# Kernel tuning notes

Hardware: AMD Instinct MI355X
Metric: run time of the kernel (lower is better)

Reference implementation:

```python
import jax, jax.numpy as jnp
import numpy as np

NQ, NK = 32, 128          # block height / width (AF3 local attention)
INF = 1.0e9
EPS = 1e-5


def _ln(x, w=None, b=None):
    m = jnp.mean(x, axis=-1, keepdims=True)
    v = jnp.var(x, axis=-1, keepdims=True)
    y = (x - m) * jax.lax.rsqrt(v + EPS)
    if w is not None:
        y = y * w
    if b is not None:
        y = y + b
    return y


def _key_idx(N):
    # For query block i, keys cover a window of NK atoms centered on the block.
    nb = N // NQ
    start = np.arange(nb)[:, None] * NQ - (NK - NQ) // 2
    idx = start + np.arange(NK)[None, :]          # [nb, NK]
    valid = ((idx >= 0) & (idx < N)).astype(np.float32)
    return np.clip(idx, 0, N - 1), valid


def setup_inputs() -> dict:
    key = jax.random.key(0)
    ks = iter(jax.random.split(key, 32))
    B, N, C, CZ, H, CH, CS = 4, 8192, 128, 16, 4, 32, 128
    nb = N // NQ
    nrm = lambda sh, sc=0.02: jax.random.normal(next(ks), sh, jnp.float32) * sc
    return dict(
        a=nrm((B, N, C), 1.0),
        z=nrm((B, nb, NQ, NK, CZ), 1.0),
        s=nrm((B, N, CS), 1.0),
        mask=jnp.ones((B, N), jnp.float32),
        ln_s_q_w=jnp.ones((CS,), jnp.float32),
        Wg_q=nrm((CS, C)), bg_q=jnp.zeros((C,), jnp.float32), Wb_q=nrm((CS, C)),
        ln_s_k_w=jnp.ones((CS,), jnp.float32),
        Wg_k=nrm((CS, C)), bg_k=jnp.zeros((C,), jnp.float32), Wb_k=nrm((CS, C)),
        ln_z_w=jnp.ones((CZ,), jnp.float32), ln_z_b=jnp.zeros((CZ,), jnp.float32),
        W_z=nrm((CZ, H)),
        Wq=nrm((C, H * CH)), Wk=nrm((C, H * CH)), Wv=nrm((C, H * CH)),
        Wg=nrm((C, H * CH)), bg=jnp.ones((H * CH,), jnp.float32),
        Wo=nrm((H * CH, C)), bo=jnp.zeros((C,), jnp.float32),
        W_ado=nrm((CS, C)), b_ado=jnp.full((C,), -2.0, jnp.float32),
    )


def reference(a, z, s, mask,
              ln_s_q_w, Wg_q, bg_q, Wb_q,
              ln_s_k_w, Wg_k, bg_k, Wb_k,
              ln_z_w, ln_z_b, W_z,
              Wq, Wk, Wv, Wg, bg, Wo, bo,
              W_ado, b_ado):
    B, N, C = a.shape
    H = W_z.shape[1]
    CH = Wq.shape[1] // H
    nb = N // NQ
    idx, valid = _key_idx(N)

    # --- block inputs ---
    a_q = a.reshape(B, nb, NQ, C)            # [B, nb, NQ, C]
    a_k = a[:, idx]                          # [B, nb, NK, C]
    q_mask = mask.reshape(B, nb, NQ)
    k_mask = mask[:, idx] * valid            # [B, nb, NK]
    pair_mask = q_mask[..., :, None] * k_mask[..., None, :]   # [B, nb, NQ, NK]
    mask_bias = (INF * (pair_mask - 1.0))[..., None, :, :]     # [B, nb, 1, NQ, NK]

    # --- pair bias from z ---
    zb = _ln(z, ln_z_w, ln_z_b) @ W_z        # [B, nb, NQ, NK, H]
    zb = jnp.moveaxis(zb, -1, -3)            # [B, nb, H, NQ, NK]

    # --- AdaLN conditioning ---
    s_q = s.reshape(B, nb, NQ, -1)
    s_k = s[:, idx]
    sqn = _ln(s_q, ln_s_q_w)
    skn = _ln(s_k, ln_s_k_w)
    aq = jax.nn.sigmoid(sqn @ Wg_q + bg_q) * _ln(a_q) + sqn @ Wb_q
    ak = jax.nn.sigmoid(skn @ Wg_k + bg_k) * _ln(a_k) + skn @ Wb_k

    # --- blocked attention with pair bias ---
    scale = 1.0 / np.sqrt(CH).astype(np.float32)
    q = (aq @ Wq).reshape(B, nb, NQ, H, CH) * scale
    k = (ak @ Wk).reshape(B, nb, NK, H, CH)
    v = (ak @ Wv).reshape(B, nb, NK, H, CH)
    logits = jnp.einsum('bnqhc,bnkhc->bnhqk', q, k) + mask_bias + zb
    attn = jax.nn.softmax(logits, axis=-1)
    o = jnp.einsum('bnhqk,bnkhc->bnqhc', attn, v)
    g = jax.nn.sigmoid(aq @ Wg + bg).reshape(B, nb, NQ, H, CH)
    o = (g * o).reshape(B, nb, NQ, H * CH)
    out = (o @ Wo + bo).reshape(B, N, C)[:, :N, :]

    # --- AdaLN-Zero output gate ---
    out = jax.nn.sigmoid(s @ W_ado + b_ado) * out
    return out
```

## Files before the change

### kernel.cpp

```cpp
#include <hip/hip_runtime.h>
#include <cstdint>
#include <cstddef>

#define B_ 4
#define N_ 8192
#define C_ 128
#define NB_ 256
#define EPS_ 1e-5f

typedef unsigned int u32;
typedef unsigned short u16;

typedef short bf16x8 __attribute__((ext_vector_type(8)));
typedef float f32x4 __attribute__((ext_vector_type(4)));
union U16x8 { uint4 u4; bf16x8 v; };

__device__ __forceinline__ float bf2f(u16 v){ union{u32 i; float f;} x; x.i = ((u32)v)<<16; return x.f; }
__device__ __forceinline__ u16 f2bf(float f){ union{float f; u32 i;} x; x.f=f; u32 r = x.i + 0x7fffu + ((x.i>>16)&1u); return (u16)(r>>16); }
__device__ __forceinline__ u32 pk2(float a, float b){ return (u32)f2bf(a) | ((u32)f2bf(b)<<16); }
__device__ __forceinline__ float sigm(float x){ return 1.f/(1.f+__expf(-x)); }

__global__ void k0_prep(const float* __restrict__ Wgq, const float* __restrict__ Wbq,
                        const float* __restrict__ Wgk, const float* __restrict__ Wbk,
                        const float* __restrict__ Wado, const float* __restrict__ Wq_,
                        const float* __restrict__ Wg_, const float* __restrict__ Wk_,
                        const float* __restrict__ Wv_, const float* __restrict__ Wo_,
                        const float* __restrict__ lnsqw, const float* __restrict__ lnskw,
                        const float* __restrict__ lnzw, const float* __restrict__ lnzb,
                        const float* __restrict__ Wz,
                        u16* __restrict__ PW, float* __restrict__ AUX)
{
  if (blockIdx.x < 80) {
    int gid = blockIdx.x*256 + threadIdx.x;
    int mat = gid >> 11;
    int rem = gid & 2047;
    int ks = rem >> 9;
    int rem2 = rem & 511;
    int nt = rem2 >> 6;
    int lane = rem2 & 63;
    int kbase = ks*32 + (lane>>4)*8;
    int n = nt*16 + (lane&15);
    const float* W; int scmode = 0; float fixed = 1.f;
    switch (mat) {
      case 0: W = Wgq; scmode = 1; break;
      case 1: W = Wbq; scmode = 1; break;
      case 2: W = Wgk; scmode = 2; break;
      case 3: W = Wbk; scmode = 2; break;
      case 4: W = Wado; break;
      case 5: W = Wq_; fixed = 0.17677669529663687f; break;
      case 6: W = Wg_; break;
      case 7: W = Wk_; break;
      case 8: W = Wv_; break;
      default: W = Wo_; break;
    }
    u16 o[8];
    #pragma unroll
    for (int j=0;j<8;j++){
      int k = kbase + j;
      float sc = fixed;
      if (scmode == 1) sc *= lnsqw[k];
      else if (scmode == 2) sc *= lnskw[k];
      o[j] = f2bf(W[k*128 + n] * sc);
    }
    uint4 pk;
    pk.x = (u32)o[0] | ((u32)o[1]<<16); pk.y = (u32)o[2] | ((u32)o[3]<<16);
    pk.z = (u32)o[4] | ((u32)o[5]<<16); pk.w = (u32)o[6] | ((u32)o[7]<<16);
    *(uint4*)(PW + (size_t)gid*8) = pk;
  } else {
    int t = threadIdx.x;
    if (t < 128) {
      float s = 0.f;
      for (int k=0;k<128;k++) s += Wado[k*128 + t];
      AUX[t] = s;
    } else if (t < 192) {
      int h = (t-128) >> 4, c = (t-128) & 15;
      AUX[t] = lnzw[c] * Wz[c*4 + h];
    } else if (t < 196) {
      int h = t - 192;
      float s = 0.f;
      for (int c=0;c<16;c++) s += lnzb[c]*Wz[c*4 + h];
      AUX[t] = s;
    }
  }
}

__device__ __forceinline__ void mm_single(f32x4 acc[4][2], const u16* Abase, const u16* __restrict__ PW,
                                          int mat, int wave, int lane, int lq, int quad)
{
  #pragma unroll
  for (int ks=0; ks<4; ks++){
    U16x8 b0, b1;
    b0.u4 = *(const uint4*)(PW + (size_t)((((mat*4+ks)*8) + wave*2+0)*64 + lane)*8);
    b1.u4 = *(const uint4*)(PW + (size_t)((((mat*4+ks)*8) + wave*2+1)*64 + lane)*8);
    #pragma unroll
    for (int mt=0; mt<4; mt++){
      U16x8 a; a.u4 = *(const uint4*)(Abase + (mt*16+lq)*136 + ks*32 + quad*8);
      acc[mt][0] = __builtin_amdgcn_mfma_f32_16x16x32_bf16(a.v, b0.v, acc[mt][0], 0,0,0);
      acc[mt][1] = __builtin_amdgcn_mfma_f32_16x16x32_bf16(a.v, b1.v, acc[mt][1], 0,0,0);
    }
  }
}
__device__ __forceinline__ void mm_dual(f32x4 acc1[4][2], int m1, f32x4 acc2[4][2], int m2,
                                        const u16* Abase, const u16* __restrict__ PW,
                                        int wave, int lane, int lq, int quad)
{
  #pragma unroll
  for (int ks=0; ks<4; ks++){
    U16x8 b10, b11, b20, b21;
    b10.u4 = *(const uint4*)(PW + (size_t)((((m1*4+ks)*8) + wave*2+0)*64 + lane)*8);
    b11.u4 = *(const uint4*)(PW + (size_t)((((m1*4+ks)*8) + wave*2+1)*64 + lane)*8);
    b20.u4 = *(const uint4*)(PW + (size_t)((((m2*4+ks)*8) + wave*2+0)*64 + lane)*8);
    b21.u4 = *(const uint4*)(PW + (size_t)((((m2*4+ks)*8) + wave*2+1)*64 + lane)*8);
    #pragma unroll
    for (int mt=0; mt<4; mt++){
      U16x8 a; a.u4 = *(const uint4*)(Abase + (mt*16+lq)*136 + ks*32 + quad*8);
      acc1[mt][0] = __builtin_amdgcn_mfma_f32_16x16x32_bf16(a.v, b10.v, acc1[mt][0], 0,0,0);
      acc1[mt][1] = __builtin_amdgcn_mfma_f32_16x16x32_bf16(a.v, b11.v, acc1[mt][1], 0,0,0);
      acc2[mt][0] = __builtin_amdgcn_mfma_f32_16x16x32_bf16(a.v, b20.v, acc2[mt][0], 0,0,0);
      acc2[mt][1] = __builtin_amdgcn_mfma_f32_16x16x32_bf16(a.v, b21.v, acc2[mt][1], 0,0,0);
    }
  }
}
#define ZERO82(A) do{ _Pragma("unroll") for(int _m=0;_m<4;_m++){ A[_m][0]=(f32x4)(0.f); A[_m][1]=(f32x4)(0.f);} }while(0)

__global__ __launch_bounds__(256, 2)
void k1_proj(const float* __restrict__ ga, const float* __restrict__ gs,
             const float* __restrict__ bgq, const float* __restrict__ bgk,
             const float* __restrict__ bg, const float* __restrict__ bado,
             const u16* __restrict__ PW, const float* __restrict__ AUX,
             u16* __restrict__ Q, u16* __restrict__ K, u16* __restrict__ VT,
             u16* __restrict__ GT, u16* __restrict__ ADO)
{
  __shared__ char arena[52736];
  u16* SN  = (u16*)arena;
  u16* LNA = (u16*)(arena + 17408);
  u16* AQ  = (u16*)(arena + 34816);
  float* SSTAT = (float*)(arena + 52224);

  const int tid = (int)threadIdx.x;
  const int rowbase = (int)blockIdx.x * 64;
  const int b = rowbase >> 13;
  const int nb0 = rowbase & 8191;
  const int wave = tid >> 6, lane = tid & 63;
  const int lq = lane & 15, quad = lane >> 4;

  {
    const float* sbase = gs + (size_t)rowbase*128;
    const float* abase = ga + (size_t)rowbase*128;
    #pragma unroll 1
    for (int t=0;t<8;t++){
      int chunk = t*256 + tid;
      int row = chunk >> 5;
      int k4 = (chunk & 31) * 4;
      float4 vs = *(const float4*)(sbase + (size_t)chunk*4);
      float4 va = *(const float4*)(abase + (size_t)chunk*4);
      float sm = vs.x+vs.y+vs.z+vs.w, sq = vs.x*vs.x+vs.y*vs.y+vs.z*vs.z+vs.w*vs.w;
      float am = va.x+va.y+va.z+va.w, a2 = va.x*va.x+va.y*va.y+va.z*va.z+va.w*va.w;
      #pragma unroll
      for (int m=1;m<32;m<<=1){
        sm += __shfl_xor(sm,m,32); sq += __shfl_xor(sq,m,32);
        am += __shfl_xor(am,m,32); a2 += __shfl_xor(a2,m,32);
      }
      float smean = sm*(1.f/128.f);
      float svar  = sq*(1.f/128.f) - smean*smean;
      float srstd = rsqrtf(svar + EPS_);
      float amean = am*(1.f/128.f);
      float avar  = a2*(1.f/128.f) - amean*amean;
      float arstd = rsqrtf(avar + EPS_);
      *(uint2*)(SN + row*136 + k4) = make_uint2(
        pk2((vs.x-smean)*srstd,(vs.y-smean)*srstd), pk2((vs.z-smean)*srstd,(vs.w-smean)*srstd));
      *(uint2*)(LNA + row*136 + k4) = make_uint2(
        pk2((va.x-amean)*arstd,(va.y-amean)*arstd), pk2((va.z-amean)*arstd,(va.w-amean)*arstd));
      if ((tid & 31) == 0){
        SSTAT[row*2]   = smean;
        SSTAT[row*2+1] = (svar + EPS_)*srstd;
      }
    }
  }
  __syncthreads();

  const int cg0 = wave*32 + lq;
  const int cg1 = cg0 + 16;

  {
    f32x4 acc[4][2]; ZERO82(acc);
    mm_single(acc, SN, PW, 4, wave, lane, lq, quad);
    float cs0 = AUX[cg0], cs1 = AUX[cg1];
    float bb0 = bado[cg0], bb1 = bado[cg1];
    #pragma unroll
    for (int mt=0; mt<4; mt++){
      #pragma unroll
      for (int reg=0; reg<4; reg++){
        int row = mt*16 + quad*4 + reg;
        float mean = SSTAT[row*2], std = SSTAT[row*2+1];
        ADO[(size_t)(rowbase+row)*128 + cg0] = f2bf(sigm(std*acc[mt][0][reg] + mean*cs0 + bb0));
        ADO[(size_t)(rowbase+row)*128 + cg1] = f2bf(sigm(std*acc[mt][1][reg] + mean*cs1 + bb1));
      }
    }
  }

  {
    f32x4 aG[4][2], aB[4][2]; ZERO82(aG); ZERO82(aB);
    mm_dual(aG, 0, aB, 1, SN, PW, wave, lane, lq, quad);
    float bq0 = bgq[cg0], bq1 = bgq[cg1];
    #pragma unroll
    for (int mt=0; mt<4; mt++){
      #pragma unroll
      for (int reg=0; reg<4; reg++){
        int row = mt*16 + quad*4 + reg;
        float l0 = bf2f(LNA[row*136 + cg0]), l1 = bf2f(LNA[row*136 + cg1]);
        AQ[row*136 + cg0] = f2bf(sigm(aG[mt][0][reg]+bq0)*l0 + aB[mt][0][reg]);
        AQ[row*136 + cg1] = f2bf(sigm(aG[mt][1][reg]+bq1)*l1 + aB[mt][1][reg]);
      }
    }
  }

  {
    f32x4 aG[4][2], aB[4][2]; ZERO82(aG); ZERO82(aB);
    mm_dual(aG, 2, aB, 3, SN, PW, wave, lane, lq, quad);
    float bk0 = bgk[cg0], bk1 = bgk[cg1];
    #pragma unroll
    for (int mt=0; mt<4; mt++){
      #pragma unroll
      for (int reg=0; reg<4; reg++){
        int row = mt*16 + quad*4 + reg;
        float l0 = bf2f(LNA[row*136 + cg0]), l1 = bf2f(LNA[row*136 + cg1]);
        aG[mt][0][reg] = sigm(aG[mt][0][reg]+bk0)*l0 + aB[mt][0][reg];
        aG[mt][1][reg] = sigm(aG[mt][1][reg]+bk1)*l1 + aB[mt][1][reg];
      }
    }
    __syncthreads();
    #pragma unroll
    for (int mt=0; mt<4; mt++){
      #pragma unroll
      for (int reg=0; reg<4; reg++){
        int row = mt*16 + quad*4 + reg;
        SN[row*136 + cg0] = f2bf(aG[mt][0][reg]);
        SN[row*136 + cg1] = f2bf(aG[mt][1][reg]);
      }
    }
    __syncthreads();
  }

  {
    f32x4 aQ_[4][2], aG_[4][2]; ZERO82(aQ_); ZERO82(aG_);
    mm_dual(aQ_, 5, aG_, 6, AQ, PW, wave, lane, lq, quad);
    float bg0 = bg[cg0], bg1 = bg[cg1];
    #pragma unroll
    for (int mt=0; mt<4; mt++){
      #pragma unroll
      for (int reg=0; reg<4; reg++){
        int row = mt*16 + quad*4 + reg;
        Q[(size_t)(rowbase+row)*128 + cg0] = f2bf(aQ_[mt][0][reg]);
        Q[(size_t)(rowbase+row)*128 + cg1] = f2bf(aQ_[mt][1][reg]);
      }
      ushort4 p0, p1;
      p0.x = f2bf(sigm(aG_[mt][0][0]+bg0)); p0.y = f2bf(sigm(aG_[mt][0][1]+bg0));
      p0.z = f2bf(sigm(aG_[mt][0][2]+bg0)); p0.w = f2bf(sigm(aG_[mt][0][3]+bg0));
      p1.x = f2bf(sigm(aG_[mt][1][0]+bg1)); p1.y = f2bf(sigm(aG_[mt][1][1]+bg1));
      p1.z = f2bf(sigm(aG_[mt][1][2]+bg1)); p1.w = f2bf(sigm(aG_[mt][1][3]+bg1));
      int nloc = nb0 + mt*16 + quad*4;
      *(ushort4*)(GT + ((size_t)(b*128 + cg0))*N_ + nloc) = p0;
      *(ushort4*)(GT + ((size_t)(b*128 + cg1))*N_ + nloc) = p1;
    }
  }

  {
    f32x4 aK_[4][2], aV_[4][2]; ZERO82(aK_); ZERO82(aV_);
    mm_dual(aK_, 7, aV_, 8, SN, PW, wave, lane, lq, quad);
    #pragma unroll
    for (int mt=0; mt<4; mt++){
      #pragma unroll
      for (int reg=0; reg<4; reg++){
        int row = mt*16 + quad*4 + reg;
        K[(size_t)(rowbase+row)*128 + cg0] = f2bf(aK_[mt][0][reg]);
        K[(size_t)(rowbase+row)*128 + cg1] = f2bf(aK_[mt][1][reg]);
      }
      ushort4 p0, p1;
      p0.x = f2bf(aV_[mt][0][0]); p0.y = f2bf(aV_[mt][0][1]);
      p0.z = f2bf(aV_[mt][0][2]); p0.w = f2bf(aV_[mt][0][3]);
      p1.x = f2bf(aV_[mt][1][0]); p1.y = f2bf(aV_[mt][1][1]);
      p1.z = f2bf(aV_[mt][1][2]); p1.w = f2bf(aV_[mt][1][3]);
      int nloc = nb0 + mt*16 + quad*4;
      *(ushort4*)(VT + ((size_t)(b*128 + cg0))*N_ + nloc) = p0;
      *(ushort4*)(VT + ((size_t)(b*128 + cg1))*N_ + nloc) = p1;
    }
  }
}

__global__ __launch_bounds__(256, 3)
void k2_attn(const float* __restrict__ gz, const float* __restrict__ gmask,
             const float* __restrict__ bo,
             const u16* __restrict__ PW, const float* __restrict__ AUX,
             const u16* __restrict__ Q, const u16* __restrict__ K,
             const u16* __restrict__ VT, const u16* __restrict__ GT,
             const u16* __restrict__ ADO, float* __restrict__ gout)
{
  __shared__ char arena[44160];
  u16* ATTall = (u16*)arena;
  u16* GO     = (u16*)(arena + 34816);
  float* KMV  = (float*)(arena + 43520);
  float* QM   = (float*)(arena + 44032);

  const int i = (int)blockIdx.x, b = (int)blockIdx.y;
  const int tid = (int)threadIdx.x;
  const int wave = tid >> 6, lane = tid & 63;
  const int lq = lane & 15, quad = lane >> 4;
  const int h = wave;
  const int start = i*32 - 48;
  u16* ATT = ATTall + h*(32*136);

  if (tid < 128) {
    int raw = start + tid;
    int g = min(max(raw,0), N_-1);
    KMV[tid] = ((raw >= 0 && raw < N_) ? 1.f : 0.f) * gmask[(size_t)b*N_ + g];
  } else if (tid < 160) {
    QM[tid-128] = gmask[(size_t)b*N_ + i*32 + (tid-128)];
  }
  __syncthreads();

  f32x4 L[2][8];
  #pragma unroll
  for (int mt=0;mt<2;mt++) for (int nt=0;nt<8;nt++) L[mt][nt] = (f32x4)(0.f);
  {
    U16x8 aQ[2];
    #pragma unroll
    for (int mt=0;mt<2;mt++)
      aQ[mt].u4 = *(const uint4*)(Q + ((size_t)b*N_ + i*32 + mt*16 + lq)*128 + h*32 + quad*8);
    #pragma unroll
    for (int nt=0;nt<8;nt++){
      int kr = min(max(start + nt*16 + lq, 0), N_-1);
      U16x8 bk; bk.u4 = *(const uint4*)(K + ((size_t)b*N_ + kr)*128 + h*32 + quad*8);
      L[0][nt] = __builtin_amdgcn_mfma_f32_16x16x32_bf16(aQ[0].v, bk.v, L[0][nt], 0,0,0);
      L[1][nt] = __builtin_amdgcn_mfma_f32_16x16x32_bf16(aQ[1].v, bk.v, L[1][nt], 0,0,0);
    }
  }

  {
    float wz[16]; float wzt = 0.f;
    #pragma unroll
    for (int c=0;c<16;c++){ wz[c] = AUX[128 + h*16 + c]; wzt += wz[c]; }
    float wzc = AUX[192 + h];
    float kmvv[8];
    #pragma unroll
    for (int nt=0;nt<8;nt++) kmvv[nt] = KMV[nt*16 + lq];
    const float* zb0 = gz + (size_t)(b*NB_ + i)*32*128*16;
    #pragma unroll
    for (int mt=0;mt<2;mt++){
      #pragma unroll 1
      for (int reg=0;reg<4;reg++){
        int q = mt*16 + quad*4 + reg;
        float qm = QM[q];
        const float* zq = zb0 + (size_t)q*128*16 + lq*16;
        #pragma unroll 2
        for (int nt=0;nt<8;nt++){
          const float* zp = zq + nt*16*16;
          float4 z0 = *(const float4*)(zp);
          float4 z1 = *(const float4*)(zp+4);
          float4 z2 = *(const float4*)(zp+8);
          float4 z3 = *(const float4*)(zp+12);
          float zv[16] = {z0.x,z0.y,z0.z,z0.w, z1.x,z1.y,z1.z,z1.w,
                          z2.x,z2.y,z2.z,z2.w, z3.x,z3.y,z3.z,z3.w};
          float sm=0.f, sq=0.f, S=0.f;
          #pragma unroll
          for (int c=0;c<16;c++){ sm += zv[c]; sq = fmaf(zv[c],zv[c],sq); S = fmaf(zv[c],wz[c],S); }
          float mz = sm*(1.f/16.f);
          float rz = rsqrtf(sq*(1.f/16.f) - mz*mz + EPS_);
          float bias = 1000000000.0f*(qm*kmvv[nt] - 1.f);
          L[mt][nt][reg] += (S - mz*wzt)*rz + wzc + bias;
        }
      }
    }
  }

  #pragma unroll
  for (int mt=0;mt<2;mt++){
    #pragma unroll
    for (int reg=0;reg<4;reg++){
      float mx = -3.0e38f;
      #pragma unroll
      for (int nt=0;nt<8;nt++) mx = fmaxf(mx, L[mt][nt][reg]);
      mx = fmaxf(mx, __shfl_xor(mx,1,16));
      mx = fmaxf(mx, __shfl_xor(mx,2,16));
      mx = fmaxf(mx, __shfl_xor(mx,4,16));
      mx = fmaxf(mx, __shfl_xor(mx,8,16));
      float e[8]; float s = 0.f;
      #pragma unroll
      for (int nt=0;nt<8;nt++){ e[nt] = __expf(L[mt][nt][reg]-mx); s += e[nt]; }
      s += __shfl_xor(s,1,16);
      s += __shfl_xor(s,2,16);
      s += __shfl_xor(s,4,16);
      s += __shfl_xor(s,8,16);
      float inv = 1.f/s;
      int q = mt*16 + quad*4 + reg;
      #pragma unroll
      for (int nt=0;nt<8;nt++) ATT[q*136 + nt*16 + lq] = f2bf(e[nt]*inv);
    }
  }

  f32x4 O[2][2];
  O[0][0]=(f32x4)(0.f); O[0][1]=(f32x4)(0.f); O[1][0]=(f32x4)(0.f); O[1][1]=(f32x4)(0.f);
  #pragma unroll
  for (int ks=0;ks<4;ks++){
    U16x8 ba[2];
    #pragma unroll
    for (int nt=0;nt<2;nt++)
      ba[nt].u4 = *(const uint4*)(ATT + (nt*16+lq)*136 + ks*32 + quad*8);
    int kk = start + ks*32 + quad*8;
    kk = min(max(kk,0), N_-8);
    #pragma unroll
    for (int mt=0;mt<2;mt++){
      U16x8 av;
      av.u4 = *(const uint4*)(VT + ((size_t)(b*128 + h*32 + mt*16 + lq))*N_ + kk);
      O[mt][0] = __builtin_amdgcn_mfma_f32_16x16x32_bf16(av.v, ba[0].v, O[mt][0], 0,0,0);
      O[mt][1] = __builtin_amdgcn_mfma_f32_16x16x32_bf16(av.v, ba[1].v, O[mt][1], 0,0,0);
    }
  }

  #pragma unroll
  for (int mt=0;mt<2;mt++){
    #pragma unroll
    for (int nt=0;nt<2;nt++){
      int q = nt*16 + lq;
      int cb = h*32 + mt*16 + quad*4;
      float g0 = bf2f(GT[((size_t)(b*128 + cb+0))*N_ + i*32 + q]);
      float g1 = bf2f(GT[((size_t)(b*128 + cb+1))*N_ + i*32 + q]);
      float g2 = bf2f(GT[((size_t)(b*128 + cb+2))*N_ + i*32 + q]);
      float g3 = bf2f(GT[((size_t)(b*128 + cb+3))*N_ + i*32 + q]);
      ushort4 p;
      p.x = f2bf(g0*O[mt][nt][0]); p.y = f2bf(g1*O[mt][nt][1]);
      p.z = f2bf(g2*O[mt][nt][2]); p.w = f2bf(g3*O[mt][nt][3]);
      *(ushort4*)(GO + q*136 + cb) = p;
    }
  }
  __syncthreads();

  {
    f32x4 U[2][2];
    U[0][0]=(f32x4)(0.f); U[0][1]=(f32x4)(0.f); U[1][0]=(f32x4)(0.f); U[1][1]=(f32x4)(0.f);
    #pragma unroll
    for (int ks=0;ks<4;ks++){
      U16x8 b0, b1;
      b0.u4 = *(const uint4*)(PW + (size_t)((((9*4+ks)*8) + wave*2+0)*64 + lane)*8);
      b1.u4 = *(const uint4*)(PW + (size_t)((((9*4+ks)*8) + wave*2+1)*64 + lane)*8);
      #pragma unroll
      for (int mt=0;mt<2;mt++){
        U16x8 a; a.u4 = *(const uint4*)(GO + (mt*16+lq)*136 + ks*32 + quad*8);
        U[mt][0] = __builtin_amdgcn_mfma_f32_16x16x32_bf16(a.v, b0.v, U[mt][0], 0,0,0);
        U[mt][1] = __builtin_amdgcn_mfma_f32_16x16x32_bf16(a.v, b1.v, U[mt][1], 0,0,0);
      }
    }
    const int cg0 = wave*32 + lq, cg1 = cg0 + 16;
    float b00 = bo[cg0], b01 = bo[cg1];
    #pragma unroll
    for (int mt=0;mt<2;mt++){
      #pragma unroll
      for (int reg=0;reg<4;reg++){
        int q = mt*16 + quad*4 + reg;
        size_t rowoff = ((size_t)b*N_ + i*32 + q)*128;
        float ad0 = bf2f(ADO[rowoff + cg0]);
        float ad1 = bf2f(ADO[rowoff + cg1]);
        gout[rowoff + cg0] = ad0*(U[mt][0][reg] + b00);
        gout[rowoff + cg1] = ad1*(U[mt][1][reg] + b01);
      }
    }
  }
}

extern "C" void kernel_launch(void* const* d_in, const int* in_sizes, int n_in,
                              void* d_out, int out_size, void* d_ws, size_t ws_size,
                              hipStream_t stream) {
  (void)in_sizes; (void)n_in; (void)out_size; (void)ws_size;
  const float* ga    = (const float*)d_in[0];
  const float* gz    = (const float*)d_in[1];
  const float* gs    = (const float*)d_in[2];
  const float* gmask = (const float*)d_in[3];
  const float* lnsqw = (const float*)d_in[4];
  const float* Wgq   = (const float*)d_in[5];
  const float* bgq   = (const float*)d_in[6];
  const float* Wbq   = (const float*)d_in[7];
  const float* lnskw = (const float*)d_in[8];
  const float* Wgk   = (const float*)d_in[9];
  const float* bgk   = (const float*)d_in[10];
  const float* Wbk   = (const float*)d_in[11];
  const float* lnzw  = (const float*)d_in[12];
  const float* lnzb  = (const float*)d_in[13];
  const float* Wz    = (const float*)d_in[14];
  const float* Wq    = (const float*)d_in[15];
  const float* Wk    = (const float*)d_in[16];
  const float* Wv    = (const float*)d_in[17];
  const float* Wg    = (const float*)d_in[18];
  const float* bg    = (const float*)d_in[19];
  const float* Wo    = (const float*)d_in[20];
  const float* bo    = (const float*)d_in[21];
  const float* Wado  = (const float*)d_in[22];
  const float* bado  = (const float*)d_in[23];

  char* ws = (char*)d_ws;
  u16* Qb  = (u16*)(ws + 0);
  u16* Kb  = (u16*)(ws + 8388608);
  u16* VTb = (u16*)(ws + 16777216);
  u16* GTb = (u16*)(ws + 25165824);
  u16* ADOb= (u16*)(ws + 33554432);
  u16* PW  = (u16*)(ws + 41943040);
  float* AUX = (float*)(ws + 41943040 + 327680);

  k0_prep<<<81, 256, 0, stream>>>(Wgq, Wbq, Wgk, Wbk, Wado, Wq, Wg, Wk, Wv, Wo,
                                  lnsqw, lnskw, lnzw, lnzb, Wz, PW, AUX);
  k1_proj<<<512, 256, 0, stream>>>(ga, gs, bgq, bgk, bg, bado, PW, AUX,
                                   Qb, Kb, VTb, GTb, ADOb);
  k2_attn<<<dim3(NB_, B_), 256, 0, stream>>>(gz, gmask, bo, PW, AUX,
                                             Qb, Kb, VTb, GTb, ADOb, (float*)d_out);
}
```

Measured before the change: 551.8 us.

## Precompute pair bias with mask into bf16 buffer in prep kernel

Moves the z layernorm, W_z projection and mask bias out of the attention kernel into extra blocks of the prep kernel, which writes a bf16 per-head bias tensor [B,nb,H,NK,NQ]. The attention kernel then adds this bias with vectorized loads instead of re-reading 128 MB of fp32 z inside the softmax stage. The sigmoid gate is stored row-major instead of transposed, attention shared memory is reduced so occupancy can rise from 3 to 4 blocks, and the block index is remapped. The trade-off is an extra 32 MB bias write and read, plus bf16 rounding of the bias including the large mask term.

```diff
diff --git a/kernel.cpp b/kernel.cpp
--- a/kernel.cpp
+++ b/kernel.cpp
@@ -28,59 +28,113 @@
                         const float* __restrict__ lnsqw, const float* __restrict__ lnskw,
                         const float* __restrict__ lnzw, const float* __restrict__ lnzb,
                         const float* __restrict__ Wz,
-                        u16* __restrict__ PW, float* __restrict__ AUX)
+                        const float* __restrict__ gz, const float* __restrict__ gmask,
+                        u16* __restrict__ PW, float* __restrict__ AUX, u16* __restrict__ ZB)
 {
-  if (blockIdx.x < 80) {
-    int gid = blockIdx.x*256 + threadIdx.x;
-    int mat = gid >> 11;
-    int rem = gid & 2047;
-    int ks = rem >> 9;
-    int rem2 = rem & 511;
-    int nt = rem2 >> 6;
-    int lane = rem2 & 63;
-    int kbase = ks*32 + (lane>>4)*8;
-    int n = nt*16 + (lane&15);
-    const float* W; int scmode = 0; float fixed = 1.f;
-    switch (mat) {
-      case 0: W = Wgq; scmode = 1; break;
-      case 1: W = Wbq; scmode = 1; break;
-      case 2: W = Wgk; scmode = 2; break;
-      case 3: W = Wbk; scmode = 2; break;
-      case 4: W = Wado; break;
-      case 5: W = Wq_; fixed = 0.17677669529663687f; break;
-      case 6: W = Wg_; break;
-      case 7: W = Wk_; break;
-      case 8: W = Wv_; break;
-      default: W = Wo_; break;
-    }
-    u16 o[8];
-    #pragma unroll
-    for (int j=0;j<8;j++){
-      int k = kbase + j;
-      float sc = fixed;
-      if (scmode == 1) sc *= lnsqw[k];
-      else if (scmode == 2) sc *= lnskw[k];
-      o[j] = f2bf(W[k*128 + n] * sc);
-    }
-    uint4 pk;
-    pk.x = (u32)o[0] | ((u32)o[1]<<16); pk.y = (u32)o[2] | ((u32)o[3]<<16);
-    pk.z = (u32)o[4] | ((u32)o[5]<<16); pk.w = (u32)o[6] | ((u32)o[7]<<16);
-    *(uint4*)(PW + (size_t)gid*8) = pk;
-  } else {
-    int t = threadIdx.x;
-    if (t < 128) {
-      float s = 0.f;
-      for (int k=0;k<128;k++) s += Wado[k*128 + t];
-      AUX[t] = s;
-    } else if (t < 192) {
-      int h = (t-128) >> 4, c = (t-128) & 15;
-      AUX[t] = lnzw[c] * Wz[c*4 + h];
-    } else if (t < 196) {
-      int h = t - 192;
-      float s = 0.f;
-      for (int c=0;c<16;c++) s += lnzb[c]*Wz[c*4 + h];
-      AUX[t] = s;
-    }
+  __shared__ float WZL[72];
+  if (blockIdx.x < 81) {
+    if (blockIdx.x < 80) {
+      int gid = blockIdx.x*256 + threadIdx.x;
+      int mat = gid >> 11;
+      int rem = gid & 2047;
+      int ks = rem >> 9;
+      int rem2 = rem & 511;
+      int nt = rem2 >> 6;
+      int lane = rem2 & 63;
+      int kbase = ks*32 + (lane>>4)*8;
+      int n = nt*16 + (lane&15);
+      const float* W; int scmode = 0; float fixed = 1.f;
+      switch (mat) {
+        case 0: W = Wgq; scmode = 1; break;
+        case 1: W = Wbq; scmode = 1; break;
+        case 2: W = Wgk; scmode = 2; break;
+        case 3: W = Wbk; scmode = 2; break;
+        case 4: W = Wado; break;
+        case 5: W = Wq_; fixed = 0.17677669529663687f; break;
+        case 6: W = Wg_; break;
+        case 7: W = Wk_; break;
+        case 8: W = Wv_; break;
+        default: W = Wo_; break;
+      }
+      u16 o[8];
+      #pragma unroll
+      for (int j=0;j<8;j++){
+        int k = kbase + j;
+        float sc = fixed;
+        if (scmode == 1) sc *= lnsqw[k];
+        else if (scmode == 2) sc *= lnskw[k];
+        o[j] = f2bf(W[k*128 + n] * sc);
+      }
+      uint4 pk;
+      pk.x = (u32)o[0] | ((u32)o[1]<<16); pk.y = (u32)o[2] | ((u32)o[3]<<16);
+      pk.z = (u32)o[4] | ((u32)o[5]<<16); pk.w = (u32)o[6] | ((u32)o[7]<<16);
+      *(uint4*)(PW + (size_t)gid*8) = pk;
+    } else {
+      int t = threadIdx.x;
+      if (t < 128) {
+        float s = 0.f;
+        for (int k=0;k<128;k++) s += Wado[k*128 + t];
+        AUX[t] = s;
+      }
+    }
+    return;
+  }
+
+  {
+    int t = (int)threadIdx.x;
+    if (t < 64) WZL[t] = lnzw[t>>2] * Wz[t];
+    else if (t < 68) { int h = t-64; float s=0.f; for (int c=0;c<16;c++) s += lnzw[c]*Wz[c*4+h]; WZL[64+h]=s; }
+    else if (t < 72) { int h = t-68; float s=0.f; for (int c=0;c<16;c++) s += lnzb[c]*Wz[c*4+h]; WZL[68+h]=s; }
+  }
+  __syncthreads();
+
+  const int blk = (int)blockIdx.x - 81;
+  const int bi = blk >> 3;
+  const int kg = blk & 7;
+  const int b = bi >> 8, i = bi & 255;
+  const int t = (int)threadIdx.x;
+  const int q = t & 31, kl = t >> 5;
+  const int key0 = kg*16 + kl, key1 = key0 + 8;
+
+  const float* z0 = gz + (size_t)bi*65536 + ((size_t)q*128 + key0)*16;
+  const float* z1 = z0 + 8*16;
+  float4 a0 = *(const float4*)(z0);      float4 a1 = *(const float4*)(z0+4);
+  float4 a2 = *(const float4*)(z0+8);    float4 a3 = *(const float4*)(z0+12);
+  float4 c0 = *(const float4*)(z1);      float4 c1 = *(const float4*)(z1+4);
+  float4 c2 = *(const float4*)(z1+8);    float4 c3 = *(const float4*)(z1+12);
+
+  const float qm = gmask[(size_t)b*N_ + i*32 + q];
+  int raw0 = i*32 - 48 + key0;
+  int raw1 = i*32 - 48 + key1;
+  float km0 = (raw0 >= 0 && raw0 < N_) ? gmask[(size_t)b*N_ + raw0] : 0.f;
+  float km1 = (raw1 >= 0 && raw1 < N_) ? gmask[(size_t)b*N_ + raw1] : 0.f;
+  float mb0 = 1000000000.0f*(qm*km0 - 1.f);
+  float mb1 = 1000000000.0f*(qm*km1 - 1.f);
+
+  u16* zbase = ZB + (size_t)bi*16384 + q;
+  #pragma unroll
+  for (int p=0;p<2;p++){
+    float zv[16];
+    if (p==0){ zv[0]=a0.x;zv[1]=a0.y;zv[2]=a0.z;zv[3]=a0.w; zv[4]=a1.x;zv[5]=a1.y;zv[6]=a1.z;zv[7]=a1.w;
+               zv[8]=a2.x;zv[9]=a2.y;zv[10]=a2.z;zv[11]=a2.w; zv[12]=a3.x;zv[13]=a3.y;zv[14]=a3.z;zv[15]=a3.w; }
+    else     { zv[0]=c0.x;zv[1]=c0.y;zv[2]=c0.z;zv[3]=c0.w; zv[4]=c1.x;zv[5]=c1.y;zv[6]=c1.z;zv[7]=c1.w;
+               zv[8]=c2.x;zv[9]=c2.y;zv[10]=c2.z;zv[11]=c2.w; zv[12]=c3.x;zv[13]=c3.y;zv[14]=c3.z;zv[15]=c3.w; }
+    float sm=0.f, sq=0.f, S0=0.f, S1=0.f, S2=0.f, S3=0.f;
+    #pragma unroll
+    for (int c=0;c<16;c++){
+      sm += zv[c]; sq = fmaf(zv[c],zv[c],sq);
+      S0 = fmaf(zv[c], WZL[c*4+0], S0); S1 = fmaf(zv[c], WZL[c*4+1], S1);
+      S2 = fmaf(zv[c], WZL[c*4+2], S2); S3 = fmaf(zv[c], WZL[c*4+3], S3);
+    }
+    float mz = sm*(1.f/16.f);
+    float rz = rsqrtf(sq*(1.f/16.f) - mz*mz + EPS_);
+    float mb = p ? mb1 : mb0;
+    int key = p ? key1 : key0;
+    u16* zo = zbase + key*32;
+    zo[0*4096] = f2bf((S0 - mz*WZL[64])*rz + WZL[68] + mb);
+    zo[1*4096] = f2bf((S1 - mz*WZL[65])*rz + WZL[69] + mb);
+    zo[2*4096] = f2bf((S2 - mz*WZL[66])*rz + WZL[70] + mb);
+    zo[3*4096] = f2bf((S3 - mz*WZL[67])*rz + WZL[71] + mb);
   }
 }
 
@@ -129,7 +183,7 @@
              const float* __restrict__ bg, const float* __restrict__ bado,
              const u16* __restrict__ PW, const float* __restrict__ AUX,
              u16* __restrict__ Q, u16* __restrict__ K, u16* __restrict__ VT,
-             u16* __restrict__ GT, u16* __restrict__ ADO)
+             u16* __restrict__ G, u16* __restrict__ ADO)
 {
   __shared__ char arena[52736];
   u16* SN  = (u16*)arena;
@@ -253,15 +307,9 @@
         int row = mt*16 + quad*4 + reg;
         Q[(size_t)(rowbase+row)*128 + cg0] = f2bf(aQ_[mt][0][reg]);
         Q[(size_t)(rowbase+row)*128 + cg1] = f2bf(aQ_[mt][1][reg]);
-      }
-      ushort4 p0, p1;
-      p0.x = f2bf(sigm(aG_[mt][0][0]+bg0)); p0.y = f2bf(sigm(aG_[mt][0][1]+bg0));
-      p0.z = f2bf(sigm(aG_[mt][0][2]+bg0)); p0.w = f2bf(sigm(aG_[mt][0][3]+bg0));
-      p1.x = f2bf(sigm(aG_[mt][1][0]+bg1)); p1.y = f2bf(sigm(aG_[mt][1][1]+bg1));
-      p1.z = f2bf(sigm(aG_[mt][1][2]+bg1)); p1.w = f2bf(sigm(aG_[mt][1][3]+bg1));
-      int nloc = nb0 + mt*16 + quad*4;
-      *(ushort4*)(GT + ((size_t)(b*128 + cg0))*N_ + nloc) = p0;
-      *(ushort4*)(GT + ((size_t)(b*128 + cg1))*N_ + nloc) = p1;
+        G[(size_t)(rowbase+row)*128 + cg0] = f2bf(sigm(aG_[mt][0][reg]+bg0));
+        G[(size_t)(rowbase+row)*128 + cg1] = f2bf(sigm(aG_[mt][1][reg]+bg1));
+      }
     }
   }
 
@@ -288,21 +336,23 @@
   }
 }
 
-__global__ __launch_bounds__(256, 3)
-void k2_attn(const float* __restrict__ gz, const float* __restrict__ gmask,
-             const float* __restrict__ bo,
-             const u16* __restrict__ PW, const float* __restrict__ AUX,
+__global__ __launch_bounds__(256, 4)
+void k2_attn(const float* __restrict__ bo,
+             const u16* __restrict__ PW,
              const u16* __restrict__ Q, const u16* __restrict__ K,
-             const u16* __restrict__ VT, const u16* __restrict__ GT,
-             const u16* __restrict__ ADO, float* __restrict__ gout)
+             const u16* __restrict__ VT, const u16* __restrict__ G,
+             const u16* __restrict__ ADO, const u16* __restrict__ ZB,
+             float* __restrict__ gout)
 {
-  __shared__ char arena[44160];
+  __shared__ char arena[34816];
   u16* ATTall = (u16*)arena;
-  u16* GO     = (u16*)(arena + 34816);
-  float* KMV  = (float*)(arena + 43520);
-  float* QM   = (float*)(arena + 44032);
-
-  const int i = (int)blockIdx.x, b = (int)blockIdx.y;
+  u16* GO     = (u16*)arena;
+
+  const int flat = (int)blockIdx.x;
+  const int x = flat & 7, r = flat >> 3;
+  const int j = r & 31, b = r >> 5;
+  const int i = x*32 + j;
+
   const int tid = (int)threadIdx.x;
   const int wave = tid >> 6, lane = tid & 63;
   const int lq = lane & 15, quad = lane >> 4;
@@ -310,15 +360,6 @@
   const int start = i*32 - 48;
   u16* ATT = ATTall + h*(32*136);
 
-  if (tid < 128) {
-    int raw = start + tid;
-    int g = min(max(raw,0), N_-1);
-    KMV[tid] = ((raw >= 0 && raw < N_) ? 1.f : 0.f) * gmask[(size_t)b*N_ + g];
-  } else if (tid < 160) {
-    QM[tid-128] = gmask[(size_t)b*N_ + i*32 + (tid-128)];
-  }
-  __syncthreads();
-
   f32x4 L[2][8];
   #pragma unroll
   for (int mt=0;mt<2;mt++) for (int nt=0;nt<8;nt++) L[mt][nt] = (f32x4)(0.f);
@@ -337,38 +378,14 @@
   }
 
   {
-    float wz[16]; float wzt = 0.f;
-    #pragma unroll
-    for (int c=0;c<16;c++){ wz[c] = AUX[128 + h*16 + c]; wzt += wz[c]; }
-    float wzc = AUX[192 + h];
-    float kmvv[8];
-    #pragma unroll
-    for (int nt=0;nt<8;nt++) kmvv[nt] = KMV[nt*16 + lq];
-    const float* zb0 = gz + (size_t)(b*NB_ + i)*32*128*16;
-    #pragma unroll
-    for (int mt=0;mt<2;mt++){
-      #pragma unroll 1
-      for (int reg=0;reg<4;reg++){
-        int q = mt*16 + quad*4 + reg;
-        float qm = QM[q];
-        const float* zq = zb0 + (size_t)q*128*16 + lq*16;
-        #pragma unroll 2
-        for (int nt=0;nt<8;nt++){
-          const float* zp = zq + nt*16*16;
-          float4 z0 = *(const float4*)(zp);
-          float4 z1 = *(const float4*)(zp+4);
-          float4 z2 = *(const float4*)(zp+8);
-          float4 z3 = *(const float4*)(zp+12);
-          float zv[16] = {z0.x,z0.y,z0.z,z0.w, z1.x,z1.y,z1.z,z1.w,
-                          z2.x,z2.y,z2.z,z2.w, z3.x,z3.y,z3.z,z3.w};
-          float sm=0.f, sq=0.f, S=0.f;
-          #pragma unroll
-          for (int c=0;c<16;c++){ sm += zv[c]; sq = fmaf(zv[c],zv[c],sq); S = fmaf(zv[c],wz[c],S); }
-          float mz = sm*(1.f/16.f);
-          float rz = rsqrtf(sq*(1.f/16.f) - mz*mz + EPS_);
-          float bias = 1000000000.0f*(qm*kmvv[nt] - 1.f);
-          L[mt][nt][reg] += (S - mz*wzt)*rz + wzc + bias;
-        }
+    const u16* zbb = ZB + (size_t)(b*NB_ + i)*16384 + h*4096;
+    #pragma unroll
+    for (int nt=0;nt<8;nt++){
+      #pragma unroll
+      for (int mt=0;mt<2;mt++){
+        ushort4 z4 = *(const ushort4*)(zbb + (nt*16+lq)*32 + mt*16 + quad*4);
+        L[mt][nt][0] += bf2f(z4.x); L[mt][nt][1] += bf2f(z4.y);
+        L[mt][nt][2] += bf2f(z4.z); L[mt][nt][3] += bf2f(z4.w);
       }
     }
   }
@@ -416,6 +433,7 @@
       O[mt][1] = __builtin_amdgcn_mfma_f32_16x16x32_bf16(av.v, ba[1].v, O[mt][1], 0,0,0);
     }
   }
+  __syncthreads();
 
   #pragma unroll
   for (int mt=0;mt<2;mt++){
@@ -423,13 +441,10 @@
     for (int nt=0;nt<2;nt++){
       int q = nt*16 + lq;
       int cb = h*32 + mt*16 + quad*4;
-      float g0 = bf2f(GT[((size_t)(b*128 + cb+0))*N_ + i*32 + q]);
-      float g1 = bf2f(GT[((size_t)(b*128 + cb+1))*N_ + i*32 + q]);
-      float g2 = bf2f(GT[((size_t)(b*128 + cb+2))*N_ + i*32 + q]);
-      float g3 = bf2f(GT[((size_t)(b*128 + cb+3))*N_ + i*32 + q]);
+      ushort4 g4 = *(const ushort4*)(G + ((size_t)b*N_ + i*32 + q)*128 + cb);
       ushort4 p;
-      p.x = f2bf(g0*O[mt][nt][0]); p.y = f2bf(g1*O[mt][nt][1]);
-      p.z = f2bf(g2*O[mt][nt][2]); p.w = f2bf(g3*O[mt][nt][3]);
+      p.x = f2bf(bf2f(g4.x)*O[mt][nt][0]); p.y = f2bf(bf2f(g4.y)*O[mt][nt][1]);
+      p.z = f2bf(bf2f(g4.z)*O[mt][nt][2]); p.w = f2bf(bf2f(g4.w)*O[mt][nt][3]);
       *(ushort4*)(GO + q*136 + cb) = p;
     }
   }
@@ -500,15 +515,16 @@
   u16* Qb  = (u16*)(ws + 0);
   u16* Kb  = (u16*)(ws + 8388608);
   u16* VTb = (u16*)(ws + 16777216);
-  u16* GTb = (u16*)(ws + 25165824);
+  u16* Gb  = (u16*)(ws + 25165824);
   u16* ADOb= (u16*)(ws + 33554432);
-  u16* PW  = (u16*)(ws + 41943040);
-  float* AUX = (float*)(ws + 41943040 + 327680);
-
-  k0_prep<<<81, 256, 0, stream>>>(Wgq, Wbq, Wgk, Wbk, Wado, Wq, Wg, Wk, Wv, Wo,
-                                  lnsqw, lnskw, lnzw, lnzb, Wz, PW, AUX);
+  u16* ZBb = (u16*)(ws + 41943040);
+  u16* PW  = (u16*)(ws + 75497472);
+  float* AUX = (float*)(ws + 75497472 + 327680);
+
+  k0_prep<<<81 + 8192, 256, 0, stream>>>(Wgq, Wbq, Wgk, Wbk, Wado, Wq, Wg, Wk, Wv, Wo,
+                                         lnsqw, lnskw, lnzw, lnzb, Wz, gz, gmask,
+                                         PW, AUX, ZBb);
   k1_proj<<<512, 256, 0, stream>>>(ga, gs, bgq, bgk, bg, bado, PW, AUX,
-                                   Qb, Kb, VTb, GTb, ADOb);
-  k2_attn<<<dim3(NB_, B_), 256, 0, stream>>>(gz, gmask, bo, PW, AUX,
-                                             Qb, Kb, VTb, GTb, ADOb, (float*)d_out);
+                                   Qb, Kb, VTb, Gb, ADOb);
+  k2_attn<<<1024, 256, 0, stream>>>(bo, PW, Qb, Kb, VTb, Gb, ADOb, ZBb, (float*)d_out);
 }
```

Result: faster. 463.7 us (-16.0%).
